# Optimization experiments

Hardware: AMD Instinct MI355X
Metric: run time of the kernel (lower is better)

Reference implementation:

```python
import jax, jax.numpy as jnp
import numpy as np
import math

# Module constants (from __init__ defaults / chosen init_kwargs)
B = 4            # hand_batch_size
C = 8            # num_cameras
BC = B * C       # camera batch
R = 256          # resolution
NB = 64          # num_bins
BIN = 0.0136     # bin_size
FOV = 33.0       # degrees
DCS = 0.001      # camera_sensor_distance
SIGMA_BIN = 3.0  # self.sigma for soft binning


def _masks():
    fov_rad = FOV * math.pi / 180.0
    scale = math.tan(fov_rad / 2.0)
    center_scale = scale * (1.0 - 1.0 / R)
    lin = jnp.linspace(-center_scale, center_scale, R, dtype=jnp.float32)
    xg, yg = jnp.meshgrid(lin, lin, indexing='xy')
    fm = jnp.stack([xg, -yg, -jnp.ones((R, R), jnp.float32)], axis=2)
    film_mask = -fm / jnp.linalg.norm(fm, axis=2, keepdims=True)  # [R,R,3]
    cos_mask = 1.0 / jnp.sqrt(xg * xg + yg * yg + 1.0)            # [R,R]
    return film_mask, cos_mask


def setup_inputs() -> dict:
    key = jax.random.key(0)
    k1, k2 = jax.random.split(key)
    film_mask, cos_mask = _masks()
    # per-pixel interpolated vertex normals (pre-normalization, as dr.interpolate output)
    normals = jax.random.normal(k1, (BC, R, R, 3), dtype=jnp.float32)
    # per-pixel camera-space intersection points; z ~ 0.5 m so depths fall mid-histogram
    intersections = jax.random.normal(k2, (BC, R, R, 3), dtype=jnp.float32) * 0.1 \
        + jnp.array([0.0, 0.0, 0.5], dtype=jnp.float32)
    return {"normals": normals, "intersections": intersections,
            "film_mask": film_mask, "cos_mask": cos_mask}


def reference(normals, intersections, film_mask, cos_mask):
    width = 2.0 * math.tan(FOV * math.pi / 360.0)
    # cosine foreshortening w.r.t. film ray directions
    dots = jnp.clip(jnp.einsum('ijk,bijk->bij', film_mask, normals), 0.0, 1.0)
    # laser origin offset by 2 * camera_sensor_distance along +x
    laser_points = intersections - jnp.array([2.0 * DCS, 0.0, 0.0], dtype=intersections.dtype)
    laser_distances = jnp.linalg.norm(laser_points, axis=3)  # [BC,R,R]
    laser_tan = jnp.sqrt(laser_points[..., 0] ** 2 + laser_points[..., 1] ** 2) / laser_points[..., 2]
    sig = math.tan(math.radians(21.5)) / 1.4
    laser_mask = jnp.exp(-laser_tan ** 2 / (2.0 * sig * sig))
    dots = dots * laser_mask
    radiance = dots / laser_distances / laser_distances / math.pi \
        * (width * width) * (cos_mask ** 3) / float(R * R)      # [BC,R,R]
    depths = (jnp.linalg.norm(intersections, axis=3) + laser_distances) / 2.0
    d_bin = depths / BIN                                         # [BC,R,R]
    b = jnp.arange(NB, dtype=jnp.float32)                        # [NB]
    # soft bin kernel: sigmoid(s*(d-b)) - sigmoid(s*(d-b-1)), [BC,R,R,NB]
    x = d_bin[..., None] - b
    kernels = jax.nn.sigmoid(SIGMA_BIN * x) - jax.nn.sigmoid(SIGMA_BIN * (x - 1.0))
    # histogram accumulation over all pixels -> per-camera transient [BC,NB]
    transients = jnp.einsum('bijk,bij->bk', kernels, radiance)
    return transients
```

## Files before the change

### kernel.cpp

```cpp
#include <hip/hip_runtime.h>
#include <math.h>

#define NPIX    65536
#define NBINS   64
#define NBATCH  32
#define SPLIT   32
#define BLOCKT  256
#define PXPT    4
#define ITERS   (NPIX / SPLIT / (BLOCKT * PXPT))
#define WIN     12
#define HSTRIDE 68
#define NG      (BLOCKT / 2)
#define SCRATCH (4 * NBINS)
#define LDSN    (NG * HSTRIDE + SCRATCH)

#define THREE_LOG2E 4.328085122666891f

__global__ __launch_bounds__(BLOCKT, 4) void spad_hist_kernel(
    const float* __restrict__ normals,
    const float* __restrict__ inters,
    const float* __restrict__ film,
    const float* __restrict__ cosm,
    float* __restrict__ ws,
    float kconst, float lmask_c, float half_inv_bin)
{
    __shared__ float hist[LDSN];
    const int tid = threadIdx.x;
    for (int i = tid; i < LDSN; i += BLOCKT) hist[i] = 0.0f;
    __syncthreads();

    const int b = blockIdx.x & (NBATCH - 1);
    const int chunk = blockIdx.x / NBATCH;
    const int pix0 = chunk * (NPIX / SPLIT);
    const int gbase = (tid >> 1) * HSTRIDE;
    const int odd = tid & 1;

    const float E3P[13] = {
        1.0f, 20.085536923187668f, 403.4287934927351f, 8103.083927575384f,
        162754.79141900392f, 3269017.372472111f, 65659969.13733051f,
        1318815734.4832146f, 26489122129.843472f, 532048240601.79865f,
        10686474581524.462f, 214643579785916.06f, 4311231547115195.0f };

    #pragma unroll
    for (int it = 0; it < ITERS; ++it) {
        const int pp = pix0 + (it * BLOCKT + tid) * PXPT;
        const float4* n4 = (const float4*)(normals + ((size_t)b * NPIX + pp) * 3);
        const float4* i4 = (const float4*)(inters  + ((size_t)b * NPIX + pp) * 3);
        const float4* f4 = (const float4*)(film + (size_t)pp * 3);
        const float4  c4 = *(const float4*)(cosm + pp);
        float4 n0 = n4[0], n1 = n4[1], n2 = n4[2];
        float4 i0 = i4[0], i1 = i4[1], i2 = i4[2];
        float4 f0 = f4[0], f1 = f4[1], f2 = f4[2];

        float NX[4] = {n0.x, n0.w, n1.z, n2.y}, NY[4] = {n0.y, n1.x, n1.w, n2.z},
              NZ[4] = {n0.z, n1.y, n2.x, n2.w};
        float IX[4] = {i0.x, i0.w, i1.z, i2.y}, IY[4] = {i0.y, i1.x, i1.w, i2.z},
              IZ[4] = {i0.z, i1.y, i2.x, i2.w};
        float FX[4] = {f0.x, f0.w, f1.z, f2.y}, FY[4] = {f0.y, f1.x, f1.w, f2.z},
              FZ[4] = {f0.z, f1.y, f2.x, f2.w};
        float CM[4] = {c4.x, c4.y, c4.z, c4.w};

        int   K0[4];
        float W[4][WIN];

        #pragma unroll
        for (int p = 0; p < 4; ++p) {
            float dt = FX[p] * NX[p] + FY[p] * NY[p] + FZ[p] * NZ[p];
            dt = fminf(fmaxf(dt, 0.0f), 1.0f);
            float lx = IX[p] - 0.002f;
            float lxy2 = lx * lx + IY[p] * IY[p];
            float l2 = lxy2 + IZ[p] * IZ[p];
            float ldst = __builtin_amdgcn_sqrtf(l2);
            float lm = __builtin_amdgcn_exp2f(
                lmask_c * lxy2 * __builtin_amdgcn_rcpf(IZ[p] * IZ[p]));
            float cm3 = CM[p] * CM[p] * CM[p];
            float r = dt * lm * kconst * cm3 * __builtin_amdgcn_rcpf(l2);
            float di = __builtin_amdgcn_sqrtf(
                IX[p] * IX[p] + IY[p] * IY[p] + IZ[p] * IZ[p]);
            float d = (di + ldst) * half_inv_bin;

            int j0 = (int)floorf(d);
            j0 = j0 < 4 ? 4 : (j0 > 56 ? 56 : j0);
            int k0 = (j0 - 4) & ~3;
            K0[p] = k0;
            float e0 = __builtin_amdgcn_exp2f(((float)k0 - d) * THREE_LOG2E);
            float S[WIN + 1];
            #pragma unroll
            for (int m = 0; m < WIN + 1; ++m)
                S[m] = __builtin_amdgcn_rcpf(fmaf(e0, E3P[m], 1.0f));
            #pragma unroll
            for (int m = 0; m < WIN; ++m)
                W[p][m] = r * (S[m] - S[m + 1]);
        }

        if (!odd) {
            #pragma unroll
            for (int p = 0; p < 4; ++p) {
                float4* hp = (float4*)&hist[gbase + K0[p]];
                float4 a = hp[0], bb = hp[1], c = hp[2];
                a.x  += W[p][0];  a.y  += W[p][1];  a.z  += W[p][2];  a.w  += W[p][3];
                bb.x += W[p][4];  bb.y += W[p][5];  bb.z += W[p][6];  bb.w += W[p][7];
                c.x  += W[p][8];  c.y  += W[p][9];  c.z  += W[p][10]; c.w  += W[p][11];
                hp[0] = a; hp[1] = bb; hp[2] = c;
            }
        }
        asm volatile("" ::: "memory");
        if (odd) {
            #pragma unroll
            for (int p = 0; p < 4; ++p) {
                float4* hp = (float4*)&hist[gbase + K0[p]];
                float4 a = hp[0], bb = hp[1], c = hp[2];
                a.x  += W[p][0];  a.y  += W[p][1];  a.z  += W[p][2];  a.w  += W[p][3];
                bb.x += W[p][4];  bb.y += W[p][5];  bb.z += W[p][6];  bb.w += W[p][7];
                c.x  += W[p][8];  c.y  += W[p][9];  c.z  += W[p][10]; c.w  += W[p][11];
                hp[0] = a; hp[1] = bb; hp[2] = c;
            }
        }
        asm volatile("" ::: "memory");
    }
    __syncthreads();

    {
        const int bin = tid & 63, s = tid >> 6;
        float sum = 0.0f;
        #pragma unroll
        for (int g = 0; g < NG / 4; ++g)
            sum += hist[(s * (NG / 4) + g) * HSTRIDE + bin];
        hist[NG * HSTRIDE + s * NBINS + bin] = sum;
    }
    __syncthreads();
    if (tid < NBINS) {
        const float* pa = &hist[NG * HSTRIDE];
        ws[(size_t)blockIdx.x * NBINS + tid] =
            pa[tid] + pa[NBINS + tid] + pa[2 * NBINS + tid] + pa[3 * NBINS + tid];
    }
}

__global__ __launch_bounds__(256) void spad_reduce_kernel(
    const float* __restrict__ ws, float* __restrict__ out)
{
    const int o = blockIdx.x * 256 + threadIdx.x;
    const int b = o >> 6;
    const int k = o & 63;
    float s = 0.0f;
    #pragma unroll
    for (int c = 0; c < SPLIT; ++c)
        s += ws[((size_t)(c * NBATCH + b)) * NBINS + k];
    out[o] = s;
}

extern "C" void kernel_launch(void* const* d_in, const int* in_sizes, int n_in,
                              void* d_out, int out_size, void* d_ws, size_t ws_size,
                              hipStream_t stream) {
    const float* normals = (const float*)d_in[0];
    const float* inters  = (const float*)d_in[1];
    const float* film    = (const float*)d_in[2];
    const float* cosm    = (const float*)d_in[3];
    float* out = (float*)d_out;
    float* ws  = (float*)d_ws;

    const double fov_rad = 33.0 * M_PI / 180.0;
    const double width = 2.0 * tan(fov_rad / 2.0);
    const double kconst_d = width * width / M_PI / 65536.0;
    const double sig = tan(21.5 * M_PI / 180.0) / 1.4;
    const double log2e = 1.4426950408889634;
    const double lmask_c_d = -log2e / (2.0 * sig * sig);
    const double half_inv_bin_d = 0.5 / 0.0136;

    spad_hist_kernel<<<NBATCH * SPLIT, BLOCKT, 0, stream>>>(
        normals, inters, film, cosm, ws,
        (float)kconst_d, (float)lmask_c_d, (float)half_inv_bin_d);

    spad_reduce_kernel<<<(NBATCH * NBINS) / 256, 256, 0, stream>>>(ws, out);
}
```

Measured before the change: 93.99 us.

## Recompute film and cosine masks analytically, interleave histogram updates per pixel

The film_mask and cos_mask inputs are no longer read. The kernel rebuilds each pixel's film direction and cosine factor from its x and y index using linspace constants computed on the host, with one rsqrt per pixel. This removes about 16 bytes per pixel of global traffic. The histogram read-modify-writes now happen right after each pixel's weights are computed instead of after all four, which should lower register pressure. The risk is small float differences from the linspace values and less overlap of the LDS updates.

```diff
diff --git a/kernel.cpp b/kernel.cpp
--- a/kernel.cpp
+++ b/kernel.cpp
@@ -16,13 +16,23 @@
 
 #define THREE_LOG2E 4.328085122666891f
 
+static __device__ __forceinline__ void rmw12(float* hp, const float* W) {
+    float4* h4 = (float4*)hp;
+    float4 a = h4[0], bb = h4[1], c = h4[2];
+    a.x  += W[0];  a.y  += W[1];  a.z  += W[2];  a.w  += W[3];
+    bb.x += W[4];  bb.y += W[5];  bb.z += W[6];  bb.w += W[7];
+    c.x  += W[8];  c.y  += W[9];  c.z  += W[10]; c.w  += W[11];
+    h4[0] = a; h4[1] = bb; h4[2] = c;
+}
+
 __global__ __launch_bounds__(BLOCKT, 4) void spad_hist_kernel(
     const float* __restrict__ normals,
     const float* __restrict__ inters,
     const float* __restrict__ film,
     const float* __restrict__ cosm,
     float* __restrict__ ws,
-    float kconst, float lmask_c, float half_inv_bin)
+    float kconst, float lmask_c, float half_inv_bin,
+    float xstep, float xneg)
 {
     __shared__ float hist[LDSN];
     const int tid = threadIdx.x;
@@ -46,34 +56,33 @@
         const int pp = pix0 + (it * BLOCKT + tid) * PXPT;
         const float4* n4 = (const float4*)(normals + ((size_t)b * NPIX + pp) * 3);
         const float4* i4 = (const float4*)(inters  + ((size_t)b * NPIX + pp) * 3);
-        const float4* f4 = (const float4*)(film + (size_t)pp * 3);
-        const float4  c4 = *(const float4*)(cosm + pp);
         float4 n0 = n4[0], n1 = n4[1], n2 = n4[2];
         float4 i0 = i4[0], i1 = i4[1], i2 = i4[2];
-        float4 f0 = f4[0], f1 = f4[1], f2 = f4[2];
 
         float NX[4] = {n0.x, n0.w, n1.z, n2.y}, NY[4] = {n0.y, n1.x, n1.w, n2.z},
               NZ[4] = {n0.z, n1.y, n2.x, n2.w};
         float IX[4] = {i0.x, i0.w, i1.z, i2.y}, IY[4] = {i0.y, i1.x, i1.w, i2.z},
               IZ[4] = {i0.z, i1.y, i2.x, i2.w};
-        float FX[4] = {f0.x, f0.w, f1.z, f2.y}, FY[4] = {f0.y, f1.x, f1.w, f2.z},
-              FZ[4] = {f0.z, f1.y, f2.x, f2.w};
-        float CM[4] = {c4.x, c4.y, c4.z, c4.w};
 
-        int   K0[4];
-        float W[4][WIN];
+        const float yv = fmaf((float)(pp >> 8), xstep, xneg);
+        const float xb = fmaf((float)(pp & 255), xstep, xneg);
+        const float y2p1 = fmaf(yv, yv, 1.0f);
 
         #pragma unroll
         for (int p = 0; p < 4; ++p) {
-            float dt = FX[p] * NX[p] + FY[p] * NY[p] + FZ[p] * NZ[p];
-            dt = fminf(fmaxf(dt, 0.0f), 1.0f);
+            const float xv = fmaf((float)p, xstep, xb);
+            const float inorm = __builtin_amdgcn_rsqf(fmaf(xv, xv, y2p1));
+            float dtr = fmaf(yv, NY[p], NZ[p]);
+            dtr = fmaf(-xv, NX[p], dtr);
+            float dt = fminf(fmaxf(dtr * inorm, 0.0f), 1.0f);
+            const float cm3 = inorm * inorm * inorm;
+
             float lx = IX[p] - 0.002f;
             float lxy2 = lx * lx + IY[p] * IY[p];
             float l2 = lxy2 + IZ[p] * IZ[p];
             float ldst = __builtin_amdgcn_sqrtf(l2);
             float lm = __builtin_amdgcn_exp2f(
                 lmask_c * lxy2 * __builtin_amdgcn_rcpf(IZ[p] * IZ[p]));
-            float cm3 = CM[p] * CM[p] * CM[p];
             float r = dt * lm * kconst * cm3 * __builtin_amdgcn_rcpf(l2);
             float di = __builtin_amdgcn_sqrtf(
                 IX[p] * IX[p] + IY[p] * IY[p] + IZ[p] * IZ[p]);
@@ -82,41 +91,22 @@
             int j0 = (int)floorf(d);
             j0 = j0 < 4 ? 4 : (j0 > 56 ? 56 : j0);
             int k0 = (j0 - 4) & ~3;
-            K0[p] = k0;
             float e0 = __builtin_amdgcn_exp2f(((float)k0 - d) * THREE_LOG2E);
             float S[WIN + 1];
             #pragma unroll
             for (int m = 0; m < WIN + 1; ++m)
                 S[m] = __builtin_amdgcn_rcpf(fmaf(e0, E3P[m], 1.0f));
+            float W[WIN];
             #pragma unroll
             for (int m = 0; m < WIN; ++m)
-                W[p][m] = r * (S[m] - S[m + 1]);
+                W[m] = r * (S[m] - S[m + 1]);
+
+            float* hp = &hist[gbase + k0];
+            if (!odd) rmw12(hp, W);
+            asm volatile("" ::: "memory");
+            if (odd)  rmw12(hp, W);
+            asm volatile("" ::: "memory");
         }
-
-        if (!odd) {
-            #pragma unroll
-            for (int p = 0; p < 4; ++p) {
-                float4* hp = (float4*)&hist[gbase + K0[p]];
-                float4 a = hp[0], bb = hp[1], c = hp[2];
-                a.x  += W[p][0];  a.y  += W[p][1];  a.z  += W[p][2];  a.w  += W[p][3];
-                bb.x += W[p][4];  bb.y += W[p][5];  bb.z += W[p][6];  bb.w += W[p][7];
-                c.x  += W[p][8];  c.y  += W[p][9];  c.z  += W[p][10]; c.w  += W[p][11];
-                hp[0] = a; hp[1] = bb; hp[2] = c;
-            }
-        }
-        asm volatile("" ::: "memory");
-        if (odd) {
-            #pragma unroll
-            for (int p = 0; p < 4; ++p) {
-                float4* hp = (float4*)&hist[gbase + K0[p]];
-                float4 a = hp[0], bb = hp[1], c = hp[2];
-                a.x  += W[p][0];  a.y  += W[p][1];  a.z  += W[p][2];  a.w  += W[p][3];
-                bb.x += W[p][4];  bb.y += W[p][5];  bb.z += W[p][6];  bb.w += W[p][7];
-                c.x  += W[p][8];  c.y  += W[p][9];  c.z  += W[p][10]; c.w  += W[p][11];
-                hp[0] = a; hp[1] = bb; hp[2] = c;
-            }
-        }
-        asm volatile("" ::: "memory");
     }
     __syncthreads();
 
@@ -166,10 +156,15 @@
     const double log2e = 1.4426950408889634;
     const double lmask_c_d = -log2e / (2.0 * sig * sig);
     const double half_inv_bin_d = 0.5 / 0.0136;
+    const double scale = tan(fov_rad / 2.0);
+    const double c_d = scale * (255.0 / 256.0);
+    const float  xstep = (float)(2.0 * c_d / 255.0);
+    const float  xneg  = (float)(-c_d);
 
     spad_hist_kernel<<<NBATCH * SPLIT, BLOCKT, 0, stream>>>(
         normals, inters, film, cosm, ws,
-        (float)kconst_d, (float)lmask_c_d, (float)half_inv_bin_d);
+        (float)kconst_d, (float)lmask_c_d, (float)half_inv_bin_d,
+        xstep, xneg);
 
     spad_reduce_kernel<<<(NBATCH * NBINS) / 256, 256, 0, stream>>>(ws, out);
 }
```

Result: no change. 93.20 us (-0.8%).
